# Optimization experiments

Hardware: AMD Instinct MI355X
Metric: run time of the kernel (lower is better)

## Reference

```python
import jax, jax.numpy as jnp
import numpy as np

B, T, D = 2, 2048, 4096
H, KH, HD = 32, 8, 128          # n_heads, n_kv_heads, head_dim = D // H
WINDOW, NGLOBAL = 1024, 32      # sliding window size, global sink tokens
ROPE_BASE = 500000.0


def _rope_tables(seq_len, dim):
    inv_freq = 1.0 / (ROPE_BASE ** (np.arange(0, dim, 2, dtype=np.float64) / dim))
    freqs = np.outer(np.arange(seq_len, dtype=np.float64), inv_freq)
    emb = np.concatenate([freqs, freqs], axis=-1)  # [T, HD]
    cos = jnp.asarray(np.cos(emb), dtype=jnp.float32)[None, None]  # [1,1,T,HD]
    sin = jnp.asarray(np.sin(emb), dtype=jnp.float32)[None, None]
    return cos, sin


def _window_global_mask(seq_len, window, n_global):
    i = np.arange(seq_len)[:, None]  # query pos
    j = np.arange(seq_len)[None, :]  # key pos
    causal = j <= i
    local = j > (i - window)
    global_keys = j < n_global
    return jnp.asarray(causal & (local | global_keys))[None, None]  # [1,1,T,T] bool


def rotate_half(x):
    x1, x2 = jnp.split(x, 2, axis=-1)
    return jnp.concatenate([-x2, x1], axis=-1)


def setup_inputs() -> dict:
    key = jax.random.key(0)
    kx, kq, kk, kv, ko = jax.random.split(key, 5)
    s = 1.0 / np.sqrt(D)
    x = jax.random.normal(kx, (B, T, D), dtype=jnp.float32)
    # Linear weights stored [in, out] (y = x @ W), same math as torch's x @ W.T
    Wq = jax.random.normal(kq, (D, H * HD), dtype=jnp.float32) * s
    Wk = jax.random.normal(kk, (D, KH * HD), dtype=jnp.float32) * s
    Wv = jax.random.normal(kv, (D, KH * HD), dtype=jnp.float32) * s
    Wo = jax.random.normal(ko, (H * HD, D), dtype=jnp.float32) * s
    cos, sin = _rope_tables(T, HD)
    mask = _window_global_mask(T, WINDOW, NGLOBAL)
    return {"x": x, "Wq": Wq, "Wk": Wk, "Wv": Wv, "Wo": Wo,
            "cos": cos, "sin": sin, "mask": mask}


def reference(x, Wq, Wk, Wv, Wo, cos, sin, mask):
    Bx, Tx, Dx = x.shape
    q = (x @ Wq).reshape(Bx, Tx, H, HD).transpose(0, 2, 1, 3)   # [B,H,T,HD]
    k = (x @ Wk).reshape(Bx, Tx, KH, HD).transpose(0, 2, 1, 3)  # [B,KH,T,HD]
    v = (x @ Wv).reshape(Bx, Tx, KH, HD).transpose(0, 2, 1, 3)
    # RoPE
    q = q * cos + rotate_half(q) * sin
    k = k * cos + rotate_half(k) * sin
    # GQA: repeat_interleave KV heads to match query heads (faithful to source)
    factor = H // KH
    k = jnp.repeat(k, factor, axis=1)  # [B,H,T,HD]
    v = jnp.repeat(v, factor, axis=1)
    # SDPA with dense bool mask (True = attend), default scale 1/sqrt(HD)
    scale = 1.0 / np.sqrt(HD)
    scores = jnp.einsum('bhqd,bhkd->bhqk', q, k) * scale  # [B,H,T,T]
    scores = jnp.where(mask, scores, jnp.finfo(scores.dtype).min)
    attn = jax.nn.softmax(scores, axis=-1)
    out = jnp.einsum('bhqk,bhkd->bhqd', attn, v)
    out = out.transpose(0, 2, 1, 3).reshape(Bx, Tx, H * HD)
    return out @ Wo
```

## Files before the change

### kernel.cpp

```cpp
#include <hip/hip_runtime.h>
#include <stdint.h>

typedef unsigned short u16;
typedef __bf16 bf16x8 __attribute__((ext_vector_type(8)));
typedef float f32x4 __attribute__((ext_vector_type(4)));

#define D_MODEL 4096
#define T_SEQ   2048
#define B_SZ    2
#define NH      32
#define NKV     8
#define HDIM    128
#define WINDOW  1024
#define NGLOB   32
#define QSTR    6144

static constexpr float SCALE = 0.08838834764831845f;

__device__ __forceinline__ u16 f2b(float f) {
  __bf16 h = (__bf16)f;
  return __builtin_bit_cast(u16, h);
}
__device__ __forceinline__ float b2f(u16 u) {
  return (float)__builtin_bit_cast(__bf16, u);
}

__global__ __launch_bounds__(256) void convert_bf16_kernel(const float* __restrict__ in,
                                                           u16* __restrict__ outp, int n4) {
  int i = blockIdx.x * 256 + threadIdx.x;
  if (i >= n4) return;
  float4 v = ((const float4*)in)[i];
  ushort4 o;
  o.x = f2b(v.x); o.y = f2b(v.y); o.z = f2b(v.z); o.w = f2b(v.w);
  ((ushort4*)outp)[i] = o;
}

__global__ __launch_bounds__(256) void transpose_w_kernel(const float* __restrict__ W,
                                                          u16* __restrict__ Wt, int Kd, int Nd) {
  __shared__ float tile[32][33];
  int tx = threadIdx.x & 31, ty = threadIdx.x >> 5;
  int bx = blockIdx.x * 32;
  int by = blockIdx.y * 32;
#pragma unroll
  for (int i = 0; i < 4; ++i)
    tile[ty + i * 8][tx] = W[(size_t)(by + ty + i * 8) * Nd + bx + tx];
  __syncthreads();
#pragma unroll
  for (int i = 0; i < 4; ++i)
    Wt[(size_t)(bx + ty + i * 8) * Kd + by + tx] = f2b(tile[tx][ty + i * 8]);
}

__global__ __launch_bounds__(256) void transpose_v_kernel(const u16* __restrict__ in,
                                                          u16* __restrict__ outp) {
  __shared__ u16 tile[32][33];
  int tx = threadIdx.x & 31, ty = threadIdx.x >> 5;
  int x0 = blockIdx.x * 32;
  int t0 = blockIdx.y * 32;
  int b = blockIdx.z;
  const u16* src = in + (size_t)b * T_SEQ * QSTR;
  u16* dst = outp + (size_t)b * (NKV * HDIM) * T_SEQ;
#pragma unroll
  for (int i = 0; i < 4; ++i)
    tile[ty + i * 8][tx] = src[(size_t)(t0 + ty + i * 8) * QSTR + x0 + tx];
  __syncthreads();
#pragma unroll
  for (int i = 0; i < 4; ++i)
    dst[(size_t)(x0 + ty + i * 8) * T_SEQ + t0 + tx] = tile[tx][ty + i * 8];
}

template <typename CT>
__global__ __launch_bounds__(512, 2) void gemm256_kernel(const u16* __restrict__ A,
                                                         const u16* __restrict__ Bt,
                                                         CT* __restrict__ C,
                                                         int ldc, int K) {
  __shared__ u16 sh[65536];
  const int tid = threadIdx.x;
  const int wave = tid >> 6, lane = tid & 63;
  const int g = lane >> 4, li = lane & 15;
  const int wr = wave >> 2, wc = wave & 3;
  const int m0 = blockIdx.y * 256, n0 = blockIdx.x * 256;
  const int r0 = tid >> 3;
  const int cs = ((tid & 7) ^ ((tid >> 3) & 7)) << 3;
  const u16* pA = A + (size_t)(m0 + r0) * K + cs;
  const u16* pB = Bt + (size_t)(n0 + r0) * K + cs;
  const int sl0 = (g ^ (li & 7)) << 3;
  const int sl1 = ((4 + g) ^ (li & 7)) << 3;
  const int nT = K >> 6;

  f32x4 acc[8][4];
  f32x4 zz = {0.f, 0.f, 0.f, 0.f};
#pragma unroll
  for (int M = 0; M < 8; ++M)
#pragma unroll
    for (int n = 0; n < 4; ++n) acc[M][n] = zz;

  auto stage = [&](const u16* src0, int ts, int dstBase) {
#pragma unroll
    for (int i = 0; i < 2; ++i) {
      const u16* s = src0 + (size_t)(i * 64) * K + ts * 64;
      __builtin_amdgcn_global_load_lds((__attribute__((address_space(1))) void*)s,
                                       (__attribute__((address_space(3))) void*)(sh + dstBase + i * 4096 + wave * 512),
                                       16, 0, 0);
    }
  };

  stage(pA, 0, 0);
  stage(pA + (size_t)128 * K, 0, 8192);
  stage(pB, 0, 16384);
  stage(pB + (size_t)128 * K, 0, 24576);
  stage(pB, 1, 32768 + 16384);
  stage(pB + (size_t)128 * K, 1, 32768 + 24576);
  stage(pA, 1, 32768);
  asm volatile("s_waitcnt vmcnt(6)" ::: "memory");
  __builtin_amdgcn_s_barrier();

  bf16x8 afr[4][2], bfr[4][2];
  for (int t = 0; t < nT; ++t) {
    const int cur = t & 1;
    const int ab = cur * 32768, bb = ab + 16384;
    const int nb = (cur ^ 1) * 32768;
    const int tn1 = (t + 1 < nT) ? t + 1 : nT - 1;
    const int tn2 = (t + 2 < nT) ? t + 2 : nT - 1;
#pragma unroll
    for (int n = 0; n < 4; ++n) {
      int row = wc * 64 + n * 16 + li;
      bfr[n][0] = *(const bf16x8*)&sh[bb + row * 64 + sl0];
      bfr[n][1] = *(const bf16x8*)&sh[bb + row * 64 + sl1];
    }
#pragma unroll
    for (int m = 0; m < 4; ++m) {
      int row = wr * 128 + m * 16 + li;
      afr[m][0] = *(const bf16x8*)&sh[ab + row * 64 + sl0];
      afr[m][1] = *(const bf16x8*)&sh[ab + row * 64 + sl1];
    }
    stage(pA + (size_t)128 * K, tn1, nb + 8192);
    __builtin_amdgcn_s_barrier();
    asm volatile("s_waitcnt lgkmcnt(0)" ::: "memory");
    __builtin_amdgcn_sched_barrier(0);
    __builtin_amdgcn_s_setprio(1);
#pragma unroll
    for (int m = 0; m < 4; ++m)
#pragma unroll
      for (int n = 0; n < 2; ++n) {
        acc[m][n] = __builtin_amdgcn_mfma_f32_16x16x32_bf16(afr[m][0], bfr[n][0], acc[m][n], 0, 0, 0);
        acc[m][n] = __builtin_amdgcn_mfma_f32_16x16x32_bf16(afr[m][1], bfr[n][1], acc[m][n], 0, 0, 0);
      }
    __builtin_amdgcn_s_setprio(0);
    __builtin_amdgcn_s_barrier();
    stage(pB, tn2, bb);
    __builtin_amdgcn_s_barrier();
    __builtin_amdgcn_s_setprio(1);
#pragma unroll
    for (int m = 0; m < 4; ++m)
#pragma unroll
      for (int n = 2; n < 4; ++n) {
        acc[m][n] = __builtin_amdgcn_mfma_f32_16x16x32_bf16(afr[m][0], bfr[n][0], acc[m][n], 0, 0, 0);
        acc[m][n] = __builtin_amdgcn_mfma_f32_16x16x32_bf16(afr[m][1], bfr[n][1], acc[m][n], 0, 0, 0);
      }
    __builtin_amdgcn_s_setprio(0);
    __builtin_amdgcn_s_barrier();
#pragma unroll
    for (int m = 0; m < 4; ++m) {
      int row = wr * 128 + 64 + m * 16 + li;
      afr[m][0] = *(const bf16x8*)&sh[ab + row * 64 + sl0];
      afr[m][1] = *(const bf16x8*)&sh[ab + row * 64 + sl1];
    }
    stage(pB + (size_t)128 * K, tn2, bb + 8192);
    __builtin_amdgcn_s_barrier();
    asm volatile("s_waitcnt lgkmcnt(0)" ::: "memory");
    __builtin_amdgcn_sched_barrier(0);
    __builtin_amdgcn_s_setprio(1);
#pragma unroll
    for (int m = 0; m < 4; ++m)
#pragma unroll
      for (int n = 0; n < 2; ++n) {
        acc[4 + m][n] = __builtin_amdgcn_mfma_f32_16x16x32_bf16(afr[m][0], bfr[n][0], acc[4 + m][n], 0, 0, 0);
        acc[4 + m][n] = __builtin_amdgcn_mfma_f32_16x16x32_bf16(afr[m][1], bfr[n][1], acc[4 + m][n], 0, 0, 0);
      }
    __builtin_amdgcn_s_setprio(0);
    __builtin_amdgcn_s_barrier();
    stage(pA, tn2, ab);
    __builtin_amdgcn_s_barrier();
    __builtin_amdgcn_s_setprio(1);
#pragma unroll
    for (int m = 0; m < 4; ++m)
#pragma unroll
      for (int n = 2; n < 4; ++n) {
        acc[4 + m][n] = __builtin_amdgcn_mfma_f32_16x16x32_bf16(afr[m][0], bfr[n][0], acc[4 + m][n], 0, 0, 0);
        acc[4 + m][n] = __builtin_amdgcn_mfma_f32_16x16x32_bf16(afr[m][1], bfr[n][1], acc[4 + m][n], 0, 0, 0);
      }
    __builtin_amdgcn_s_setprio(0);
    asm volatile("s_waitcnt vmcnt(6)" ::: "memory");
    __builtin_amdgcn_s_barrier();
  }
#pragma unroll
  for (int M = 0; M < 8; ++M)
#pragma unroll
    for (int n = 0; n < 4; ++n)
#pragma unroll
      for (int r = 0; r < 4; ++r) {
        int row = m0 + wr * 128 + M * 16 + g * 4 + r;
        int col = n0 + wc * 64 + n * 16 + li;
        if constexpr (sizeof(CT) == 2)
          C[(size_t)row * ldc + col] = (CT)f2b(acc[M][n][r]);
        else
          C[(size_t)row * ldc + col] = acc[M][n][r];
      }
}

__global__ __launch_bounds__(256) void rope_kernel(u16* __restrict__ qkv,
                                                   const float* __restrict__ cosp,
                                                   const float* __restrict__ sinp) {
  int idx = blockIdx.x * 256 + threadIdx.x;
  int d = idx & 63;
  int rest = idx >> 6;
  int hh = rest % (NH + NKV);
  int bt = rest / (NH + NKV);
  if (bt >= B_SZ * T_SEQ) return;
  int tok = bt & (T_SEQ - 1);
  float c = cosp[tok * HDIM + d], s = sinp[tok * HDIM + d];
  u16* base = qkv + (size_t)bt * QSTR + hh * HDIM;
  float x1 = b2f(base[d]), x2 = b2f(base[d + 64]);
  base[d] = f2b(x1 * c - x2 * s);
  base[d + 64] = f2b(x2 * c + x1 * s);
}

__global__ __launch_bounds__(256) void attn_kernel(const u16* __restrict__ qp,
                                                   const u16* __restrict__ kp,
                                                   const u16* __restrict__ vtp,
                                                   u16* __restrict__ ctx) {
  __shared__ u16 Kt[64 * 128];
  __shared__ u16 Vt[128 * 64];
  __shared__ u16 Pl[4][16 * 64];
  int tid = threadIdx.x;
  int w = tid >> 6, lane = tid & 63;
  int g = lane >> 4, li = lane & 15;
  int i0 = blockIdx.x * 64;
  int h = blockIdx.y, b = blockIdx.z;
  int kh = h >> 2;
  f32x4 zz = {0.f, 0.f, 0.f, 0.f};

  bf16x8 qf[4];
  size_t qrow = (size_t)(b * T_SEQ + i0 + w * 16 + li) * QSTR + h * HDIM;
#pragma unroll
  for (int c = 0; c < 4; ++c) qf[c] = *(const bf16x8*)(qp + qrow + c * 32 + g * 8);

  f32x4 o[8];
#pragma unroll
  for (int f = 0; f < 8; ++f) o[f] = zz;
  float m_s[4] = {-1e30f, -1e30f, -1e30f, -1e30f};
  float l_s[4] = {0.f, 0.f, 0.f, 0.f};

  int jmax = i0 + 63;
  for (int j0 = 0; j0 <= jmax; j0 += 64) {
    if (!((j0 < NGLOB) || (j0 + 63 > i0 - WINDOW))) continue;
    __syncthreads();
#pragma unroll
    for (int i = 0; i < 4; ++i) {
      int o8 = tid + 256 * i;
      int krow = o8 >> 4, kch = o8 & 15;
      size_t gk = (size_t)(b * T_SEQ + j0 + krow) * QSTR + kh * HDIM + kch * 8;
      *(bf16x8*)&Kt[(krow * 128 + kch * 8) ^ ((krow & 7) << 3)] = *(const bf16x8*)(kp + gk);
      int vrow = o8 >> 3, vch = o8 & 7;
      size_t gv = ((size_t)(b * NKV + kh) * HDIM + vrow) * T_SEQ + j0 + vch * 8;
      *(bf16x8*)&Vt[(vrow * 64 + vch * 8) ^ ((vrow & 7) << 3)] = *(const bf16x8*)(vtp + gv);
    }
    __syncthreads();

    f32x4 s[4];
#pragma unroll
    for (int kb = 0; kb < 4; ++kb) s[kb] = zz;
#pragma unroll
    for (int c = 0; c < 4; ++c) {
      int hd0 = c * 32 + g * 8;
#pragma unroll
      for (int kb = 0; kb < 4; ++kb) {
        int key = kb * 16 + li;
        bf16x8 kf = *(const bf16x8*)&Kt[(key * 128 + hd0) ^ ((key & 7) << 3)];
        s[kb] = __builtin_amdgcn_mfma_f32_16x16x32_bf16(qf[c], kf, s[kb], 0, 0, 0);
      }
    }

    float corr[4];
#pragma unroll
    for (int r = 0; r < 4; ++r) {
      int irow = i0 + w * 16 + g * 4 + r;
      float x[4];
#pragma unroll
      for (int kb = 0; kb < 4; ++kb) {
        int j = j0 + kb * 16 + li;
        float xx = s[kb][r] * SCALE;
        bool vm = (j <= irow) && ((j > irow - WINDOW) || (j < NGLOB));
        x[kb] = vm ? xx : -1e30f;
      }
      float mt = fmaxf(fmaxf(x[0], x[1]), fmaxf(x[2], x[3]));
#pragma unroll
      for (int dd = 1; dd < 16; dd <<= 1) mt = fmaxf(mt, __shfl_xor(mt, dd, 64));
      float mn = fmaxf(m_s[r], mt);
      corr[r] = __expf(m_s[r] - mn);
      m_s[r] = mn;
      float rs = 0.f;
      int prow = g * 4 + r;
#pragma unroll
      for (int kb = 0; kb < 4; ++kb) {
        x[kb] = __expf(x[kb] - mn);
        rs += x[kb];
        Pl[w][(prow * 64 + kb * 16 + li) ^ ((prow & 7) << 3)] = f2b(x[kb]);
      }
#pragma unroll
      for (int dd = 1; dd < 16; dd <<= 1) rs += __shfl_xor(rs, dd, 64);
      l_s[r] = l_s[r] * corr[r] + rs;
    }
#pragma unroll
    for (int f = 0; f < 8; ++f) {
      o[f][0] *= corr[0]; o[f][1] *= corr[1];
      o[f][2] *= corr[2]; o[f][3] *= corr[3];
    }

    bf16x8 pa0 = *(const bf16x8*)&Pl[w][(li * 64 + 0 + g * 8) ^ ((li & 7) << 3)];
    bf16x8 pa1 = *(const bf16x8*)&Pl[w][(li * 64 + 32 + g * 8) ^ ((li & 7) << 3)];

#pragma unroll
    for (int f = 0; f < 8; ++f) {
      int hd = f * 16 + li;
      bf16x8 v0 = *(const bf16x8*)&Vt[(hd * 64 + 0 + g * 8) ^ ((li & 7) << 3)];
      bf16x8 v1 = *(const bf16x8*)&Vt[(hd * 64 + 32 + g * 8) ^ ((li & 7) << 3)];
      o[f] = __builtin_amdgcn_mfma_f32_16x16x32_bf16(pa0, v0, o[f], 0, 0, 0);
      o[f] = __builtin_amdgcn_mfma_f32_16x16x32_bf16(pa1, v1, o[f], 0, 0, 0);
    }
  }

#pragma unroll
  for (int f = 0; f < 8; ++f)
#pragma unroll
    for (int r = 0; r < 4; ++r) {
      size_t orow = (size_t)(b * T_SEQ + i0 + w * 16 + g * 4 + r) * (NH * HDIM) + h * HDIM + f * 16 + li;
      ctx[orow] = f2b(o[f][r] / l_s[r]);
    }
}

extern "C" void kernel_launch(void* const* d_in, const int* in_sizes, int n_in,
                              void* d_out, int out_size, void* d_ws, size_t ws_size,
                              hipStream_t stream) {
  const float* x    = (const float*)d_in[0];
  const float* Wq   = (const float*)d_in[1];
  const float* Wk   = (const float*)d_in[2];
  const float* Wv   = (const float*)d_in[3];
  const float* Wo   = (const float*)d_in[4];
  const float* cosp = (const float*)d_in[5];
  const float* sinp = (const float*)d_in[6];

  char* ws = (char*)d_ws;
  u16* xb     = (u16*)(ws + 0ull);
  u16* Wqkvt  = (u16*)(ws + 33554432ull);
  u16* Wot    = (u16*)(ws + 83886080ull);
  u16* qkv    = (u16*)(ws + 117440512ull);
  u16* ctx    = xb;
  u16* vT     = Wqkvt;

  convert_bf16_kernel<<<16384, 256, 0, stream>>>(x, xb, 4194304);
  transpose_w_kernel<<<dim3(128, 128), 256, 0, stream>>>(Wq, Wqkvt, 4096, 4096);
  transpose_w_kernel<<<dim3(32, 128), 256, 0, stream>>>(Wk, Wqkvt + (size_t)4096 * 4096, 4096, 1024);
  transpose_w_kernel<<<dim3(32, 128), 256, 0, stream>>>(Wv, Wqkvt + (size_t)5120 * 4096, 4096, 1024);
  transpose_w_kernel<<<dim3(128, 128), 256, 0, stream>>>(Wo, Wot, 4096, 4096);

  gemm256_kernel<u16><<<dim3(24, 16), 512, 0, stream>>>(xb, Wqkvt, qkv, QSTR, 4096);

  transpose_v_kernel<<<dim3(32, 64, 2), 256, 0, stream>>>(qkv + 5120, vT);

  rope_kernel<<<40960, 256, 0, stream>>>(qkv, cosp, sinp);

  attn_kernel<<<dim3(32, 32, 2), 256, 0, stream>>>(qkv, qkv + 4096, vT, ctx);

  gemm256_kernel<float><<<dim3(16, 16), 512, 0, stream>>>(ctx, Wot, (float*)d_out, 4096, 4096);
}
```

Measured before the change: 610.4 us.

## Use 256x192 tile GEMM for QKV projection and vectorize RoPE kernel

Adds a new QKV GEMM kernel with 256x192 output tiles, giving a 32x16 grid of 512 blocks instead of 24x16 = 384. With 256 CUs this evens out the wave count, where 384 blocks left half the last wave idle. The new kernel keeps the double-buffered global-to-LDS pipeline with loads interleaved between MFMA phases. It also rewrites RoPE so each thread handles 8 elements with vector bf16 and float4 loads, using 8x fewer blocks. The risks are a narrower per-wave tile, which lowers data reuse, and higher register pressure from launch_bounds(512,2).

```diff
diff --git a/kernel.cpp b/kernel.cpp
--- a/kernel.cpp
+++ b/kernel.cpp
@@ -208,21 +208,164 @@
       }
 }
 
+__global__ __launch_bounds__(512, 2) void gemm192_kernel(const u16* __restrict__ A,
+                                                         const u16* __restrict__ Bt,
+                                                         u16* __restrict__ C,
+                                                         int ldc, int K) {
+  __shared__ u16 sh[57344];
+  const int tid = threadIdx.x;
+  const int wave = tid >> 6, lane = tid & 63;
+  const int g = lane >> 4, li = lane & 15;
+  const int wr = wave >> 2, wc = wave & 3;
+  const int m0 = blockIdx.y * 256, n0 = blockIdx.x * 192;
+  const int r0 = tid >> 3;
+  const int cs = ((tid & 7) ^ ((tid >> 3) & 7)) << 3;
+  const u16* pA = A + (size_t)(m0 + r0) * K + cs;
+  const u16* pB = Bt + (size_t)(n0 + r0) * K + cs;
+  const int sl0 = (g ^ (li & 7)) << 3;
+  const int sl1 = ((4 + g) ^ (li & 7)) << 3;
+  const int nT = K >> 6;
+
+  f32x4 acc[8][3];
+  f32x4 zz = {0.f, 0.f, 0.f, 0.f};
+#pragma unroll
+  for (int M = 0; M < 8; ++M)
+#pragma unroll
+    for (int n = 0; n < 3; ++n) acc[M][n] = zz;
+
+  auto stage64 = [&](const u16* src0, int ts, int dstU16) {
+    __builtin_amdgcn_global_load_lds(
+        (__attribute__((address_space(1))) void*)(src0 + (size_t)ts * 64),
+        (__attribute__((address_space(3))) void*)(sh + dstU16 + wave * 512), 16, 0, 0);
+  };
+
+#pragma unroll
+  for (int u = 0; u < 4; ++u) stage64(pA + (size_t)(u * 64) * K, 0, u * 4096);
+#pragma unroll
+  for (int u = 0; u < 3; ++u) stage64(pB + (size_t)(u * 64) * K, 0, 16384 + u * 4096);
+#pragma unroll
+  for (int u = 0; u < 4; ++u) stage64(pA + (size_t)(u * 64) * K, 1, 28672 + u * 4096);
+#pragma unroll
+  for (int u = 0; u < 3; ++u) stage64(pB + (size_t)(u * 64) * K, 1, 28672 + 16384 + u * 4096);
+  asm volatile("s_waitcnt vmcnt(7)" ::: "memory");
+  __builtin_amdgcn_s_barrier();
+
+  bf16x8 afr[4][2], bfr[3][2];
+  for (int t = 0; t < nT; ++t) {
+    const int ab = (t & 1) * 28672, bb = ab + 16384;
+    const int tn2 = (t + 2 < nT) ? t + 2 : nT - 1;
+#pragma unroll
+    for (int n = 0; n < 3; ++n) {
+      int row = wc * 48 + n * 16 + li;
+      bfr[n][0] = *(const bf16x8*)&sh[bb + row * 64 + sl0];
+      bfr[n][1] = *(const bf16x8*)&sh[bb + row * 64 + sl1];
+    }
+#pragma unroll
+    for (int m = 0; m < 4; ++m) {
+      int row = wr * 128 + m * 16 + li;
+      afr[m][0] = *(const bf16x8*)&sh[ab + row * 64 + sl0];
+      afr[m][1] = *(const bf16x8*)&sh[ab + row * 64 + sl1];
+    }
+    __builtin_amdgcn_s_barrier();
+    asm volatile("s_waitcnt lgkmcnt(0)" ::: "memory");
+    __builtin_amdgcn_sched_barrier(0);
+    __builtin_amdgcn_s_setprio(1);
+#pragma unroll
+    for (int m = 0; m < 4; ++m)
+#pragma unroll
+      for (int n = 0; n < 2; ++n) {
+        acc[m][n] = __builtin_amdgcn_mfma_f32_16x16x32_bf16(afr[m][0], bfr[n][0], acc[m][n], 0, 0, 0);
+        acc[m][n] = __builtin_amdgcn_mfma_f32_16x16x32_bf16(afr[m][1], bfr[n][1], acc[m][n], 0, 0, 0);
+      }
+    __builtin_amdgcn_s_setprio(0);
+    __builtin_amdgcn_s_barrier();
+    stage64(pB, tn2, bb);
+    stage64(pB + (size_t)64 * K, tn2, bb + 4096);
+    stage64(pA, tn2, ab);
+    __builtin_amdgcn_s_barrier();
+    __builtin_amdgcn_s_setprio(1);
+#pragma unroll
+    for (int m = 0; m < 4; ++m) {
+      acc[m][2] = __builtin_amdgcn_mfma_f32_16x16x32_bf16(afr[m][0], bfr[2][0], acc[m][2], 0, 0, 0);
+      acc[m][2] = __builtin_amdgcn_mfma_f32_16x16x32_bf16(afr[m][1], bfr[2][1], acc[m][2], 0, 0, 0);
+    }
+    __builtin_amdgcn_s_setprio(0);
+    __builtin_amdgcn_s_barrier();
+#pragma unroll
+    for (int m = 0; m < 4; ++m) {
+      int row = wr * 128 + 64 + m * 16 + li;
+      afr[m][0] = *(const bf16x8*)&sh[ab + row * 64 + sl0];
+      afr[m][1] = *(const bf16x8*)&sh[ab + row * 64 + sl1];
+    }
+    stage64(pB + (size_t)128 * K, tn2, bb + 8192);
+    stage64(pA + (size_t)128 * K, tn2, ab + 8192);
+    __builtin_amdgcn_s_barrier();
+    asm volatile("s_waitcnt lgkmcnt(0)" ::: "memory");
+    __builtin_amdgcn_sched_barrier(0);
+    __builtin_amdgcn_s_setprio(1);
+#pragma unroll
+    for (int m = 0; m < 4; ++m)
+#pragma unroll
+      for (int n = 0; n < 2; ++n) {
+        acc[4 + m][n] = __builtin_amdgcn_mfma_f32_16x16x32_bf16(afr[m][0], bfr[n][0], acc[4 + m][n], 0, 0, 0);
+        acc[4 + m][n] = __builtin_amdgcn_mfma_f32_16x16x32_bf16(afr[m][1], bfr[n][1], acc[4 + m][n], 0, 0, 0);
+      }
+    __builtin_amdgcn_s_setprio(0);
+    __builtin_amdgcn_s_barrier();
+    stage64(pA + (size_t)64 * K, tn2, ab + 4096);
+    stage64(pA + (size_t)192 * K, tn2, ab + 12288);
+    __builtin_amdgcn_s_barrier();
+    __builtin_amdgcn_s_setprio(1);
+#pragma unroll
+    for (int m = 0; m < 4; ++m) {
+      acc[4 + m][2] = __builtin_amdgcn_mfma_f32_16x16x32_bf16(afr[m][0], bfr[2][0], acc[4 + m][2], 0, 0, 0);
+      acc[4 + m][2] = __builtin_amdgcn_mfma_f32_16x16x32_bf16(afr[m][1], bfr[2][1], acc[4 + m][2], 0, 0, 0);
+    }
+    __builtin_amdgcn_s_setprio(0);
+    asm volatile("s_waitcnt vmcnt(7)" ::: "memory");
+    __builtin_amdgcn_s_barrier();
+  }
+#pragma unroll
+  for (int M = 0; M < 8; ++M)
+#pragma unroll
+    for (int n = 0; n < 3; ++n)
+#pragma unroll
+      for (int r = 0; r < 4; ++r) {
+        int row = m0 + wr * 128 + M * 16 + g * 4 + r;
+        int col = n0 + wc * 48 + n * 16 + li;
+        C[(size_t)row * ldc + col] = f2b(acc[M][n][r]);
+      }
+}
+
 __global__ __launch_bounds__(256) void rope_kernel(u16* __restrict__ qkv,
                                                    const float* __restrict__ cosp,
                                                    const float* __restrict__ sinp) {
   int idx = blockIdx.x * 256 + threadIdx.x;
-  int d = idx & 63;
-  int rest = idx >> 6;
+  int d8 = idx & 7;
+  int rest = idx >> 3;
   int hh = rest % (NH + NKV);
   int bt = rest / (NH + NKV);
   if (bt >= B_SZ * T_SEQ) return;
   int tok = bt & (T_SEQ - 1);
-  float c = cosp[tok * HDIM + d], s = sinp[tok * HDIM + d];
+  int d0 = d8 * 8;
+  const float4* cp = (const float4*)(cosp + (size_t)tok * HDIM + d0);
+  const float4* sp = (const float4*)(sinp + (size_t)tok * HDIM + d0);
+  float4 cA = cp[0], cB = cp[1];
+  float4 sA = sp[0], sB = sp[1];
+  float cc[8] = {cA.x, cA.y, cA.z, cA.w, cB.x, cB.y, cB.z, cB.w};
+  float ss[8] = {sA.x, sA.y, sA.z, sA.w, sB.x, sB.y, sB.z, sB.w};
   u16* base = qkv + (size_t)bt * QSTR + hh * HDIM;
-  float x1 = b2f(base[d]), x2 = b2f(base[d + 64]);
-  base[d] = f2b(x1 * c - x2 * s);
-  base[d + 64] = f2b(x2 * c + x1 * s);
+  bf16x8 v1 = *(const bf16x8*)(base + d0);
+  bf16x8 v2 = *(const bf16x8*)(base + d0 + 64);
+  bf16x8 o1, o2;
+#pragma unroll
+  for (int j = 0; j < 8; ++j) {
+    float xa = (float)v1[j], xb = (float)v2[j];
+    o1[j] = (__bf16)(xa * cc[j] - xb * ss[j]);
+    o2[j] = (__bf16)(xb * cc[j] + xa * ss[j]);
+  }
+  *(bf16x8*)(base + d0) = o1;
+  *(bf16x8*)(base + d0 + 64) = o2;
 }
 
 __global__ __launch_bounds__(256) void attn_kernel(const u16* __restrict__ qp,
@@ -364,11 +507,11 @@
   transpose_w_kernel<<<dim3(32, 128), 256, 0, stream>>>(Wv, Wqkvt + (size_t)5120 * 4096, 4096, 1024);
   transpose_w_kernel<<<dim3(128, 128), 256, 0, stream>>>(Wo, Wot, 4096, 4096);
 
-  gemm256_kernel<u16><<<dim3(24, 16), 512, 0, stream>>>(xb, Wqkvt, qkv, QSTR, 4096);
+  gemm192_kernel<<<dim3(32, 16), 512, 0, stream>>>(xb, Wqkvt, qkv, QSTR, 4096);
 
   transpose_v_kernel<<<dim3(32, 64, 2), 256, 0, stream>>>(qkv + 5120, vT);
 
-  rope_kernel<<<40960, 256, 0, stream>>>(qkv, cosp, sinp);
+  rope_kernel<<<5120, 256, 0, stream>>>(qkv, cosp, sinp);
 
   attn_kernel<<<dim3(32, 32, 2), 256, 0, stream>>>(qkv, qkv + 4096, vT, ctx);
 
```

Result: faster. 577.4 us (-5.4%).
